# Performance work log

Hardware: AMD Instinct MI355X
Metric: run time of the kernel (lower is better)

## Reference

```python
import jax, jax.numpy as jnp
import numpy as np

S, N, D_IN, D_GNN, E = 8, 50000, 128, 128, 1600000


def setup_inputs() -> dict:
    key = jax.random.key(0)
    k = jax.random.split(key, 7)
    inp = jax.random.normal(k[0], (S, N, D_IN), dtype=jnp.float32)
    edge_index = jax.random.randint(k[1], (2, E), 0, N, dtype=jnp.int64)
    # SAGEConv params: lin_l (neighbor branch, with bias), lin_r (root, no bias)
    s_in = 1.0 / np.sqrt(D_IN)
    W_l = jax.random.uniform(k[2], (D_GNN, D_IN), jnp.float32, -s_in, s_in)
    b_l = jax.random.uniform(k[3], (D_GNN,), jnp.float32, -s_in, s_in)
    W_r = jax.random.uniform(k[4], (D_GNN, D_IN), jnp.float32, -s_in, s_in)
    s_g = 1.0 / np.sqrt(D_GNN)
    W_fc = jax.random.uniform(k[5], (1, D_GNN), jnp.float32, -s_g, s_g)
    b_fc = jax.random.uniform(k[6], (1,), jnp.float32, -s_g, s_g)
    return {"input": inp, "edge_index": edge_index, "W_l": W_l, "b_l": b_l,
            "W_r": W_r, "W_fc": W_fc, "b_fc": b_fc}


def reference(input, edge_index, W_l, b_l, W_r, W_fc, b_fc):
    src, dst = edge_index[0], edge_index[1]
    n = input.shape[1]
    # in-degree for mean aggregation (isolated nodes -> divide by 1, agg stays 0)
    deg = jax.ops.segment_sum(jnp.ones(src.shape[0], input.dtype), dst,
                              num_segments=n)
    deg = jnp.maximum(deg, 1.0)[:, None]

    def step(xt):  # xt: [N, D_IN]
        agg = jax.ops.segment_sum(xt[src], dst, num_segments=n) / deg
        # SAGEConv: lin_l(mean_agg) + lin_r(x)
        return agg @ W_l.T + b_l + xt @ W_r.T  # [N, D_GNN]

    xs = jax.vmap(step)(input)                   # [S, N, D_GNN]
    ys = (xs @ W_fc.T + b_fc)[..., 0]            # [S, N]
    return xs, ys
```

## Files before the change

kernel.cpp:

```cpp
#include <hip/hip_runtime.h>

#define S_STEPS 8
#define D 128

typedef __attribute__((ext_vector_type(4))) float f32x4;
typedef __attribute__((ext_vector_type(4))) short s16x4;
typedef __attribute__((ext_vector_type(8))) short s16x8;

static __device__ __forceinline__ short f2bf(float f) {
    union { float f; unsigned u; } x; x.f = f;
    unsigned r = x.u + 0x7fffu + ((x.u >> 16) & 1u);
    return (short)(r >> 16);
}

__global__ void count_kernel(const int* __restrict__ dst, int* __restrict__ cnt, int E) {
    int e = blockIdx.x * blockDim.x + threadIdx.x;
    if (e < E) atomicAdd(&cnt[dst[e]], 1);
}

__global__ void cvtw_kernel(const float* __restrict__ Wl, const float* __restrict__ Wr,
                            unsigned short* __restrict__ wbf) {
    int i = blockIdx.x * blockDim.x + threadIdx.x;
    if (i < 256 * 128) {
        int j = i >> 7, k = i & 127;
        float v = (j < 128) ? Wl[j * 128 + k] : Wr[(j - 128) * 128 + k];
        wbf[i] = (unsigned short)f2bf(v);
    }
}

__global__ void cvtwcat_kernel(const float* __restrict__ Wl, const float* __restrict__ Wr,
                               unsigned short* __restrict__ wcat) {
    int i = blockIdx.x * blockDim.x + threadIdx.x;
    if (i < 128 * 256) {
        int j = i >> 8, k = i & 255;
        float v = (k < 128) ? Wl[j * 128 + k] : Wr[j * 128 + (k - 128)];
        wcat[i] = (unsigned short)f2bf(v);
    }
}

__global__ __launch_bounds__(256) void cvtx_kernel(const float* __restrict__ x,
    unsigned short* __restrict__ xbfA, unsigned short* __restrict__ xbfB, int N)
{
    const int lane = threadIdx.x & 63;
    const int wv = threadIdx.x >> 6;
    const int node = blockIdx.x * 4 + wv;
    if (node >= N) return;
#pragma unroll
    for (int t = 0; t < S_STEPS; ++t) {
        float2 v = *(const float2*)(x + ((size_t)t * N + node) * 128 + lane * 2);
        ushort2 u;
        u.x = (unsigned short)f2bf(v.x);
        u.y = (unsigned short)f2bf(v.y);
        unsigned short* tb = (t < 4) ? xbfA : xbfB;
        *(ushort2*)(tb + ((size_t)node * 4 + (t & 3)) * 128 + lane * 2) = u;
    }
}

__global__ __launch_bounds__(1024) void scan_kernel(const int* __restrict__ cnt,
                            int* __restrict__ row_ptr,
                            int* __restrict__ fill, float* __restrict__ rdeg,
                            int N, int E) {
    __shared__ int wsum[16];
    __shared__ int woff[16];
    __shared__ int carry_s;
    const int tid = threadIdx.x;
    const int lane = tid & 63;
    const int wv = tid >> 6;
    if (tid == 0) carry_s = 0;
    __syncthreads();
    for (int base = 0; base < N; base += 1024) {
        int i = base + tid;
        int v = (i < N) ? cnt[i] : 0;
        int inc = v;
#pragma unroll
        for (int off = 1; off < 64; off <<= 1) {
            int t = __shfl_up(inc, off);
            if (lane >= off) inc += t;
        }
        if (lane == 63) wsum[wv] = inc;
        __syncthreads();
        if (wv == 0 && lane < 16) {
            int s = wsum[lane];
            int in2 = s;
#pragma unroll
            for (int off = 1; off < 16; off <<= 1) {
                int t = __shfl_up(in2, off);
                if (lane >= off) in2 += t;
            }
            woff[lane] = in2 - s;
        }
        __syncthreads();
        int carry = carry_s;
        int excl = carry + woff[wv] + inc - v;
        if (i < N) {
            row_ptr[i] = excl;
            fill[i] = excl;
            rdeg[i] = 1.0f / (float)((v > 1) ? v : 1);
        }
        __syncthreads();
        if (tid == 1023) carry_s = carry + woff[15] + inc;
        __syncthreads();
    }
    if (tid == 0) row_ptr[N] = E;
}

__global__ void fill_kernel(const int* __restrict__ src, const int* __restrict__ dst,
                            int* __restrict__ fill, int* __restrict__ eidx, int E) {
    int e = blockIdx.x * blockDim.x + threadIdx.x;
    if (e < E) {
        int p = atomicAdd(&fill[dst[e]], 1);
        eidx[p] = src[e];
    }
}

__global__ __launch_bounds__(256) void lin_kernel(const float* __restrict__ x,
    const unsigned short* __restrict__ wbf, const float* __restrict__ bl,
    unsigned short* __restrict__ hbf, float* __restrict__ outb, int N,
    int SF, int tf)
{
    __shared__ __align__(16) short As[64 * 136];
    __shared__ float bls[128];

    const int tid = threadIdx.x;
    const int row0 = blockIdx.x * 64;
    const int lane = tid & 63;
    const int w = tid >> 6;
    const int m = lane & 15;
    const int q = lane >> 4;

    s16x8 bf[4][4];
#pragma unroll
    for (int ct = 0; ct < 4; ++ct) {
#pragma unroll
        for (int kc = 0; kc < 4; ++kc) {
            int col = (w * 4 + ct) * 16 + m;
            bf[ct][kc] = *(const s16x8*)(wbf + (size_t)col * 128 + kc * 32 + q * 8);
        }
    }
    if (tid < 128) bls[tid] = bl[tid];

#pragma unroll
    for (int it = 0; it < 8; ++it) {
        int i = tid + it * 256;
        int r = i >> 5;
        int kq = i & 31;
        int grow = row0 + r;
        float4 v = make_float4(0.f, 0.f, 0.f, 0.f);
        if (grow < N) v = *(const float4*)(x + (size_t)grow * 128 + kq * 4);
        s16x4 a; a.x = f2bf(v.x); a.y = f2bf(v.y); a.z = f2bf(v.z); a.w = f2bf(v.w);
        *(s16x4*)&As[r * 136 + kq * 4] = a;
    }
    __syncthreads();

    f32x4 acc[4][4];
#pragma unroll
    for (int i = 0; i < 4; ++i)
#pragma unroll
        for (int j = 0; j < 4; ++j) acc[i][j] = (f32x4){0.f, 0.f, 0.f, 0.f};

#pragma unroll
    for (int mt = 0; mt < 4; ++mt) {
        s16x8 af[4];
#pragma unroll
        for (int kc = 0; kc < 4; ++kc)
            af[kc] = *(const s16x8*)&As[(mt * 16 + m) * 136 + kc * 32 + q * 8];
#pragma unroll
        for (int ct = 0; ct < 4; ++ct)
#pragma unroll
            for (int kc = 0; kc < 4; ++kc)
                acc[mt][ct] = __builtin_amdgcn_mfma_f32_16x16x32_bf16(
                    af[kc], bf[ct][kc], acc[mt][ct], 0, 0, 0);
    }

    const int colbase = w * 64;
#pragma unroll
    for (int mt = 0; mt < 4; ++mt) {
        const int rowbase = row0 + mt * 16 + q * 4;
#pragma unroll
        for (int ct = 0; ct < 4; ++ct) {
            int col = colbase + ct * 16 + m;
#pragma unroll
            for (int r = 0; r < 4; ++r) {
                int rr = rowbase + r;
                if (rr < N) {
                    if (col < 128) {
                        hbf[((size_t)rr * SF + tf) * 128 + col] =
                            (unsigned short)f2bf(acc[mt][ct][r]);
                    } else {
                        outb[(size_t)rr * 128 + (col - 128)] = acc[mt][ct][r] + bls[col - 128];
                    }
                }
            }
        }
    }
}

#define BF2ACC(u, j) { union { unsigned v; float f; } lo_, hi_; \
    lo_.v = (u) << 16; hi_.v = (u) & 0xffff0000u; \
    acc[j] += lo_.f; acc[(j) + 1] += hi_.f; }
#define ACC8(p, j) { BF2ACC((p).x, (j)); BF2ACC((p).y, (j) + 2); \
    BF2ACC((p).z, (j) + 4); BF2ACC((p).w, (j) + 6); }

__global__ __launch_bounds__(256) void agg4x_kernel(const unsigned short* __restrict__ xbfH,
    const int* __restrict__ row_ptr, const int* __restrict__ eidx,
    const float* __restrict__ rdeg, unsigned short* __restrict__ aggxH, int N)
{
    const int lane = threadIdx.x & 63;
    const int wv = threadIdx.x >> 6;
    const int node = blockIdx.x * 4 + wv;
    if (node >= N) return;

    const int beg = row_ptr[node];
    const int end = row_ptr[node + 1];

    float acc[8];
#pragma unroll
    for (int j = 0; j < 8; ++j) acc[j] = 0.f;

    const uint4* hb = (const uint4*)xbfH;

    int e = beg;
    for (; e + 4 <= end; e += 4) {
        int s0 = eidx[e];
        int s1 = eidx[e + 1];
        int s2 = eidx[e + 2];
        int s3 = eidx[e + 3];
        uint4 a = hb[(size_t)s0 * 64 + lane];
        uint4 b = hb[(size_t)s1 * 64 + lane];
        uint4 c = hb[(size_t)s2 * 64 + lane];
        uint4 d = hb[(size_t)s3 * 64 + lane];
        ACC8(a, 0); ACC8(b, 0); ACC8(c, 0); ACC8(d, 0);
    }
    for (; e < end; ++e) {
        int s0 = eidx[e];
        uint4 a = hb[(size_t)s0 * 64 + lane];
        ACC8(a, 0);
    }

    const float rd = rdeg[node];
    unsigned short* orow = aggxH + ((size_t)node * 4 + (lane >> 4)) * 128 + (lane & 15) * 8;
    s16x8 o;
#pragma unroll
    for (int j = 0; j < 8; ++j) o[j] = f2bf(acc[j] * rd);
    __builtin_nontemporal_store(o, (s16x8*)orow);
}

__global__ __launch_bounds__(256) void lin2_kernel(
    const unsigned short* __restrict__ aggxA, const unsigned short* __restrict__ aggxB,
    const unsigned short* __restrict__ xbfA, const unsigned short* __restrict__ xbfB,
    const unsigned short* __restrict__ wcat, const float* __restrict__ bl,
    const float* __restrict__ wfc, const float* __restrict__ bfc,
    float* __restrict__ xs, float* __restrict__ ys, int N)
{
    __shared__ __align__(16) short As[64 * 264];
    __shared__ float bls[128];
    __shared__ float wfs[128];
    __shared__ float part[4][64];

    const int tid = threadIdx.x;
    const int node0 = blockIdx.x * 8;
    const int lane = tid & 63;
    const int w = tid >> 6;
    const int m = lane & 15;
    const int q = lane >> 4;

    s16x8 bf[2][8];
#pragma unroll
    for (int ct = 0; ct < 2; ++ct) {
#pragma unroll
        for (int kc = 0; kc < 8; ++kc) {
            int col = w * 32 + ct * 16 + m;
            bf[ct][kc] = *(const s16x8*)(wcat + (size_t)col * 256 + kc * 32 + q * 8);
        }
    }
    if (tid < 128) { bls[tid] = bl[tid]; wfs[tid] = wfc[tid]; }

#pragma unroll
    for (int it = 0; it < 4; ++it) {
        int c = tid + it * 256;
        int nl = c >> 7;
        int j = c & 127;
        int t = j >> 4;
        int k16 = j & 15;
        int row = nl * 8 + t;
        int node = node0 + nl;
        s16x8 va = (s16x8){0,0,0,0,0,0,0,0};
        s16x8 vx = (s16x8){0,0,0,0,0,0,0,0};
        if (node < N) {
            const unsigned short* at = (t < 4) ? aggxA : aggxB;
            const unsigned short* xt = (t < 4) ? xbfA : xbfB;
            size_t src = ((size_t)node * 4 + (t & 3)) * 128 + k16 * 8;
            va = *(const s16x8*)(at + src);
            vx = *(const s16x8*)(xt + src);
        }
        *(s16x8*)&As[row * 264 + k16 * 8] = va;
        *(s16x8*)&As[row * 264 + 128 + k16 * 8] = vx;
    }
    __syncthreads();

    f32x4 acc[4][2];
#pragma unroll
    for (int i = 0; i < 4; ++i)
#pragma unroll
        for (int j = 0; j < 2; ++j) acc[i][j] = (f32x4){0.f, 0.f, 0.f, 0.f};

#pragma unroll
    for (int mt = 0; mt < 4; ++mt) {
        s16x8 af[8];
#pragma unroll
        for (int kc = 0; kc < 8; ++kc)
            af[kc] = *(const s16x8*)&As[(mt * 16 + m) * 264 + kc * 32 + q * 8];
#pragma unroll
        for (int ct = 0; ct < 2; ++ct)
#pragma unroll
            for (int kc = 0; kc < 8; ++kc)
                acc[mt][ct] = __builtin_amdgcn_mfma_f32_16x16x32_bf16(
                    af[kc], bf[ct][kc], acc[mt][ct], 0, 0, 0);
    }

    float pd[4][4];
#pragma unroll
    for (int i = 0; i < 4; ++i)
#pragma unroll
        for (int r = 0; r < 4; ++r) pd[i][r] = 0.f;

    const int colb = w * 32;
#pragma unroll
    for (int mt = 0; mt < 4; ++mt) {
#pragma unroll
        for (int ct = 0; ct < 2; ++ct) {
            int col = colb + ct * 16 + m;
            float blv = bls[col];
            float wfv = wfs[col];
#pragma unroll
            for (int r = 0; r < 4; ++r) {
                int row = mt * 16 + q * 4 + r;
                int node = node0 + (row >> 3);
                int t = row & 7;
                float o = acc[mt][ct][r] + blv;
                if (node < N) xs[((size_t)t * N + node) * 128 + col] = o;
                pd[mt][r] += o * wfv;
            }
        }
    }
#pragma unroll
    for (int off = 1; off < 16; off <<= 1)
#pragma unroll
        for (int mt = 0; mt < 4; ++mt)
#pragma unroll
            for (int r = 0; r < 4; ++r)
                pd[mt][r] += __shfl_xor(pd[mt][r], off);
    if (m == 0) {
#pragma unroll
        for (int mt = 0; mt < 4; ++mt)
#pragma unroll
            for (int r = 0; r < 4; ++r)
                part[w][mt * 16 + q * 4 + r] = pd[mt][r];
    }
    __syncthreads();
    if (tid < 64) {
        int row = tid;
        float v = part[0][row] + part[1][row] + part[2][row] + part[3][row] + bfc[0];
        int node = node0 + (row >> 3);
        int t = row & 7;
        if (node < N) ys[(size_t)t * N + node] = v;
    }
}

__global__ __launch_bounds__(256) void agg_kernel(const unsigned short* __restrict__ hbf,
    const int* __restrict__ row_ptr, const int* __restrict__ eidx,
    const float* __restrict__ rdeg, const float* __restrict__ wfc,
    const float* __restrict__ bfc, float* __restrict__ outb,
    float* __restrict__ ys, int N)
{
    const int lane = threadIdx.x & 63;
    const int wv = threadIdx.x >> 6;
    const int node = blockIdx.x * 4 + wv;
    if (node >= N) return;
    const int g = lane >> 4;
    const int l = lane & 15;
    const int beg = row_ptr[node];
    const int end = row_ptr[node + 1];

    float acc[8];
#pragma unroll
    for (int j = 0; j < 8; ++j) acc[j] = 0.f;

    const unsigned short* hb = hbf + l * 8;
#pragma unroll 2
    for (int e = beg + g; e < end; e += 4) {
        int s = eidx[e];
        uint4 pk = *(const uint4*)(hb + (size_t)s * 128);
        union { unsigned u; float f; } t;
        t.u = pk.x << 16;        acc[0] += t.f;
        t.u = pk.x & 0xffff0000u; acc[1] += t.f;
        t.u = pk.y << 16;        acc[2] += t.f;
        t.u = pk.y & 0xffff0000u; acc[3] += t.f;
        t.u = pk.z << 16;        acc[4] += t.f;
        t.u = pk.z & 0xffff0000u; acc[5] += t.f;
        t.u = pk.w << 16;        acc[6] += t.f;
        t.u = pk.w & 0xffff0000u; acc[7] += t.f;
    }
#pragma unroll
    for (int j = 0; j < 8; ++j) {
        acc[j] += __shfl_xor(acc[j], 16);
        acc[j] += __shfl_xor(acc[j], 32);
    }
    float ax = (g == 0) ? acc[0] : (g == 1) ? acc[2] : (g == 2) ? acc[4] : acc[6];
    float ay = (g == 0) ? acc[1] : (g == 1) ? acc[3] : (g == 2) ? acc[5] : acc[7];

    const int feat = l * 8 + g * 2;
    const float rd = rdeg[node];
    const float2 base = *(const float2*)(outb + (size_t)node * 128 + feat);
    float ox = base.x + ax * rd;
    float oy = base.y + ay * rd;
    *(float2*)(outb + (size_t)node * 128 + feat) = make_float2(ox, oy);

    const float2 wv2 = *(const float2*)(wfc + feat);
    float p = ox * wv2.x + oy * wv2.y;
#pragma unroll
    for (int off = 32; off > 0; off >>= 1) p += __shfl_down(p, off);
    if (lane == 0) ys[node] = p + bfc[0];
}

extern "C" void kernel_launch(void* const* d_in, const int* in_sizes, int n_in,
                              void* d_out, int out_size, void* d_ws, size_t ws_size,
                              hipStream_t stream)
{
    const float* x   = (const float*)d_in[0];
    const int*   ei  = (const int*)d_in[1];
    const float* Wl  = (const float*)d_in[2];
    const float* bl  = (const float*)d_in[3];
    const float* Wr  = (const float*)d_in[4];
    const float* Wfc = (const float*)d_in[5];
    const float* bfc = (const float*)d_in[6];

    const int N = in_sizes[0] / (S_STEPS * D);
    const int E = in_sizes[1] / 2;
    const int* srcp = ei;
    const int* dstp = ei + E;

    char* p = (char*)d_ws;
    auto alloc = [&](size_t bytes) {
        char* r = p;
        p += (bytes + 255) & ~(size_t)255;
        return r;
    };
    int*   cnt     = (int*)alloc((size_t)N * 4);
    int*   row_ptr = (int*)alloc((size_t)(N + 1) * 4);
    int*   fill    = (int*)alloc((size_t)N * 4);
    float* rdeg    = (float*)alloc((size_t)N * 4);
    int*   eidx    = (int*)alloc((size_t)E * 4);
    unsigned short* wmat = (unsigned short*)alloc((size_t)256 * 128 * 2);

    size_t used = (size_t)(p - (char*)d_ws);
    size_t htbl = (size_t)N * 4 * D * 2;
    bool v5 = (ws_size >= used + 4 * htbl + 4096);

    float* xs    = (float*)d_out;
    float* ysall = xs + (size_t)S_STEPS * N * D;

    (void)hipMemsetAsync(cnt, 0, (size_t)N * 4, stream);
    count_kernel<<<(E + 255) / 256, 256, 0, stream>>>(dstp, cnt, E);
    scan_kernel<<<1, 1024, 0, stream>>>(cnt, row_ptr, fill, rdeg, N, E);
    fill_kernel<<<(E + 255) / 256, 256, 0, stream>>>(srcp, dstp, fill, eidx, E);

    if (v5) {
        unsigned short* xbfA  = (unsigned short*)alloc(htbl);
        unsigned short* xbfB  = (unsigned short*)alloc(htbl);
        unsigned short* aggxA = (unsigned short*)alloc(htbl);
        unsigned short* aggxB = (unsigned short*)alloc(htbl);
        cvtwcat_kernel<<<128, 256, 0, stream>>>(Wl, Wr, wmat);
        cvtx_kernel<<<(N + 3) / 4, 256, 0, stream>>>(x, xbfA, xbfB, N);
        agg4x_kernel<<<(N + 3) / 4, 256, 0, stream>>>(xbfA, row_ptr, eidx, rdeg,
                                                      aggxA, N);
        agg4x_kernel<<<(N + 3) / 4, 256, 0, stream>>>(xbfB, row_ptr, eidx, rdeg,
                                                      aggxB, N);
        lin2_kernel<<<(N + 7) / 8, 256, 0, stream>>>(aggxA, aggxB, xbfA, xbfB,
                                                     wmat, bl, Wfc, bfc,
                                                     xs, ysall, N);
    } else {
        unsigned short* hbf = (unsigned short*)alloc((size_t)N * D * 2);
        cvtw_kernel<<<128, 256, 0, stream>>>(Wl, Wr, wmat);
        const int gl = (N + 63) / 64;
        const int ga = (N + 3) / 4;
        for (int t = 0; t < S_STEPS; ++t) {
            const float* xt = x + (size_t)t * N * D;
            float* outb = xs + (size_t)t * N * D;
            lin_kernel<<<gl, 256, 0, stream>>>(xt, wmat, bl, hbf, outb, N, 1, 0);
            agg_kernel<<<ga, 256, 0, stream>>>(hbf, row_ptr, eidx, rdeg, Wfc, bfc,
                                               outb, ysall + (size_t)t * N, N);
        }
    }
}
```

Measured before the change: 1.122 ms.

## Build CSR with two-level bucket radix sort instead of global atomics

Replaces the count/scan/fill CSR construction (per-node global atomics plus a single-block serial scan over N) with a two-pass bucket sort. Edges are histogrammed into 256-node buckets, scattered into a packed buffer using block-local atomics, and then sorted within each bucket in shared memory, which also writes row_ptr. Degree reciprocals are now computed from row_ptr inside the aggregation kernel rather than read from a separate array. The path is taken only when NB<256 and N<2^24, and it needs an extra E-sized buffer.

```diff
diff --git a/kernel.cpp b/kernel.cpp
--- a/kernel.cpp
+++ b/kernel.cpp
@@ -13,47 +13,119 @@
     return (short)(r >> 16);
 }
 
+
+__global__ __launch_bounds__(256) void bhist_kernel(const int* __restrict__ dst,
+    int* __restrict__ bhist, int E)
+{
+    __shared__ int lh[256];
+    lh[threadIdx.x] = 0;
+    __syncthreads();
+    for (int e = blockIdx.x * 256 + threadIdx.x; e < E; e += gridDim.x * 256)
+        atomicAdd(&lh[dst[e] >> 8], 1);
+    __syncthreads();
+    int v = lh[threadIdx.x];
+    if (v) atomicAdd(&bhist[threadIdx.x], v);
+}
+
+__global__ __launch_bounds__(256) void bscan_kernel(const int* __restrict__ bhist,
+    int* __restrict__ bbase, int* __restrict__ cursor, int* __restrict__ row_ptr,
+    int N, int E, int NB)
+{
+    __shared__ int wsum[4];
+    __shared__ int woff[4];
+    const int tid = threadIdx.x;
+    const int lane = tid & 63;
+    const int wv = tid >> 6;
+    int v = (tid < NB) ? bhist[tid] : 0;
+    int inc = v;
+#pragma unroll
+    for (int off = 1; off < 64; off <<= 1) {
+        int t = __shfl_up(inc, off);
+        if (lane >= off) inc += t;
+    }
+    if (lane == 63) wsum[wv] = inc;
+    __syncthreads();
+    if (tid == 0) { int s = 0; for (int k = 0; k < 4; ++k) { woff[k] = s; s += wsum[k]; } }
+    __syncthreads();
+    int excl = woff[wv] + inc - v;
+    if (tid < NB) { bbase[tid] = excl; cursor[tid] = excl; }
+    if (tid == NB) bbase[NB] = E;
+    if (tid == 0) row_ptr[N] = E;
+}
+
+__global__ __launch_bounds__(256) void scat_kernel(const int* __restrict__ src,
+    const int* __restrict__ dst, int* __restrict__ cursor,
+    unsigned* __restrict__ ebuf, int E, int len, int NB)
+{
+    __shared__ int lh[256];
+    __shared__ int lb[256];
+    const int tid = threadIdx.x;
+    const int e0 = blockIdx.x * len;
+    const int e1 = min(E, e0 + len);
+    if (e0 >= E) return;
+    lh[tid] = 0;
+    __syncthreads();
+    for (int e = e0 + tid; e < e1; e += 256)
+        atomicAdd(&lh[dst[e] >> 8], 1);
+    __syncthreads();
+    if (tid < NB) lb[tid] = lh[tid] ? atomicAdd(&cursor[tid], lh[tid]) : 0;
+    __syncthreads();
+    lh[tid] = 0;
+    __syncthreads();
+    for (int e = e0 + tid; e < e1; e += 256) {
+        int d = dst[e];
+        int b = d >> 8;
+        int off = atomicAdd(&lh[b], 1);
+        ebuf[lb[b] + off] = ((unsigned)src[e] << 8) | (unsigned)(d & 255);
+    }
+}
+
+__global__ __launch_bounds__(256) void bsort_kernel(const unsigned* __restrict__ ebuf,
+    const int* __restrict__ bbase, int* __restrict__ row_ptr,
+    int* __restrict__ eidx, int N)
+{
+    __shared__ int cnt[256];
+    __shared__ int wsum[4];
+    __shared__ int woff[4];
+    const int tid = threadIdx.x;
+    const int b = blockIdx.x;
+    const int base = bbase[b];
+    const int K = bbase[b + 1] - base;
+    cnt[tid] = 0;
+    __syncthreads();
+    for (int i = tid; i < K; i += 256)
+        atomicAdd(&cnt[ebuf[base + i] & 255], 1);
+    __syncthreads();
+    int v = cnt[tid];
+    int inc = v;
+    const int lane = tid & 63;
+    const int wv = tid >> 6;
+#pragma unroll
+    for (int off = 1; off < 64; off <<= 1) {
+        int t = __shfl_up(inc, off);
+        if (lane >= off) inc += t;
+    }
+    if (lane == 63) wsum[wv] = inc;
+    __syncthreads();
+    if (tid == 0) { int s = 0; for (int k = 0; k < 4; ++k) { woff[k] = s; s += wsum[k]; } }
+    __syncthreads();
+    int excl = woff[wv] + inc - v;
+    int node = b * 256 + tid;
+    if (node < N) row_ptr[node] = base + excl;
+    __syncthreads();
+    cnt[tid] = excl;
+    __syncthreads();
+    for (int i = tid; i < K; i += 256) {
+        unsigned u = ebuf[base + i];
+        int off = atomicAdd(&cnt[u & 255], 1);
+        eidx[base + off] = (int)(u >> 8);
+    }
+}
+
+
 __global__ void count_kernel(const int* __restrict__ dst, int* __restrict__ cnt, int E) {
     int e = blockIdx.x * blockDim.x + threadIdx.x;
     if (e < E) atomicAdd(&cnt[dst[e]], 1);
-}
-
-__global__ void cvtw_kernel(const float* __restrict__ Wl, const float* __restrict__ Wr,
-                            unsigned short* __restrict__ wbf) {
-    int i = blockIdx.x * blockDim.x + threadIdx.x;
-    if (i < 256 * 128) {
-        int j = i >> 7, k = i & 127;
-        float v = (j < 128) ? Wl[j * 128 + k] : Wr[(j - 128) * 128 + k];
-        wbf[i] = (unsigned short)f2bf(v);
-    }
-}
-
-__global__ void cvtwcat_kernel(const float* __restrict__ Wl, const float* __restrict__ Wr,
-                               unsigned short* __restrict__ wcat) {
-    int i = blockIdx.x * blockDim.x + threadIdx.x;
-    if (i < 128 * 256) {
-        int j = i >> 8, k = i & 255;
-        float v = (k < 128) ? Wl[j * 128 + k] : Wr[j * 128 + (k - 128)];
-        wcat[i] = (unsigned short)f2bf(v);
-    }
-}
-
-__global__ __launch_bounds__(256) void cvtx_kernel(const float* __restrict__ x,
-    unsigned short* __restrict__ xbfA, unsigned short* __restrict__ xbfB, int N)
-{
-    const int lane = threadIdx.x & 63;
-    const int wv = threadIdx.x >> 6;
-    const int node = blockIdx.x * 4 + wv;
-    if (node >= N) return;
-#pragma unroll
-    for (int t = 0; t < S_STEPS; ++t) {
-        float2 v = *(const float2*)(x + ((size_t)t * N + node) * 128 + lane * 2);
-        ushort2 u;
-        u.x = (unsigned short)f2bf(v.x);
-        u.y = (unsigned short)f2bf(v.y);
-        unsigned short* tb = (t < 4) ? xbfA : xbfB;
-        *(ushort2*)(tb + ((size_t)node * 4 + (t & 3)) * 128 + lane * 2) = u;
-    }
 }
 
 __global__ __launch_bounds__(1024) void scan_kernel(const int* __restrict__ cnt,
@@ -113,6 +185,46 @@
     }
 }
 
+
+__global__ void cvtw_kernel(const float* __restrict__ Wl, const float* __restrict__ Wr,
+                            unsigned short* __restrict__ wbf) {
+    int i = blockIdx.x * blockDim.x + threadIdx.x;
+    if (i < 256 * 128) {
+        int j = i >> 7, k = i & 127;
+        float v = (j < 128) ? Wl[j * 128 + k] : Wr[(j - 128) * 128 + k];
+        wbf[i] = (unsigned short)f2bf(v);
+    }
+}
+
+__global__ void cvtwcat_kernel(const float* __restrict__ Wl, const float* __restrict__ Wr,
+                               unsigned short* __restrict__ wcat) {
+    int i = blockIdx.x * blockDim.x + threadIdx.x;
+    if (i < 128 * 256) {
+        int j = i >> 8, k = i & 255;
+        float v = (k < 128) ? Wl[j * 128 + k] : Wr[j * 128 + (k - 128)];
+        wcat[i] = (unsigned short)f2bf(v);
+    }
+}
+
+__global__ __launch_bounds__(256) void cvtx_kernel(const float* __restrict__ x,
+    unsigned short* __restrict__ xbfA, unsigned short* __restrict__ xbfB, int N)
+{
+    const int lane = threadIdx.x & 63;
+    const int wv = threadIdx.x >> 6;
+    const int node = blockIdx.x * 4 + wv;
+    if (node >= N) return;
+#pragma unroll
+    for (int t = 0; t < S_STEPS; ++t) {
+        float2 v = *(const float2*)(x + ((size_t)t * N + node) * 128 + lane * 2);
+        ushort2 u;
+        u.x = (unsigned short)f2bf(v.x);
+        u.y = (unsigned short)f2bf(v.y);
+        unsigned short* tb = (t < 4) ? xbfA : xbfB;
+        *(ushort2*)(tb + ((size_t)node * 4 + (t & 3)) * 128 + lane * 2) = u;
+    }
+}
+
+
 __global__ __launch_bounds__(256) void lin_kernel(const float* __restrict__ x,
     const unsigned short* __restrict__ wbf, const float* __restrict__ bl,
     unsigned short* __restrict__ hbf, float* __restrict__ outb, int N,
@@ -203,7 +315,7 @@
 
 __global__ __launch_bounds__(256) void agg4x_kernel(const unsigned short* __restrict__ xbfH,
     const int* __restrict__ row_ptr, const int* __restrict__ eidx,
-    const float* __restrict__ rdeg, unsigned short* __restrict__ aggxH, int N)
+    unsigned short* __restrict__ aggxH, int N)
 {
     const int lane = threadIdx.x & 63;
     const int wv = threadIdx.x >> 6;
@@ -237,7 +349,8 @@
         ACC8(a, 0);
     }
 
-    const float rd = rdeg[node];
+    int deg = end - beg;
+    const float rd = 1.0f / (float)((deg > 1) ? deg : 1);
     unsigned short* orow = aggxH + ((size_t)node * 4 + (lane >> 4)) * 128 + (lane & 15) * 8;
     s16x8 o;
 #pragma unroll
@@ -446,41 +559,54 @@
         p += (bytes + 255) & ~(size_t)255;
         return r;
     };
-    int*   cnt     = (int*)alloc((size_t)N * 4);
     int*   row_ptr = (int*)alloc((size_t)(N + 1) * 4);
-    int*   fill    = (int*)alloc((size_t)N * 4);
-    float* rdeg    = (float*)alloc((size_t)N * 4);
     int*   eidx    = (int*)alloc((size_t)E * 4);
     unsigned short* wmat = (unsigned short*)alloc((size_t)256 * 128 * 2);
 
+    const int NB = (N + 255) >> 8;
     size_t used = (size_t)(p - (char*)d_ws);
     size_t htbl = (size_t)N * 4 * D * 2;
-    bool v5 = (ws_size >= used + 4 * htbl + 4096);
+    size_t radix = ((size_t)E * 4 + 256) + 3 * ((size_t)(NB + 1) * 4 + 256);
+    bool v6 = (NB >= 1) && (NB < 256) && (N < (1 << 24)) &&
+              (ws_size >= used + radix + 4 * htbl + 65536);
 
     float* xs    = (float*)d_out;
     float* ysall = xs + (size_t)S_STEPS * N * D;
 
-    (void)hipMemsetAsync(cnt, 0, (size_t)N * 4, stream);
-    count_kernel<<<(E + 255) / 256, 256, 0, stream>>>(dstp, cnt, E);
-    scan_kernel<<<1, 1024, 0, stream>>>(cnt, row_ptr, fill, rdeg, N, E);
-    fill_kernel<<<(E + 255) / 256, 256, 0, stream>>>(srcp, dstp, fill, eidx, E);
-
-    if (v5) {
+    if (v6) {
+        unsigned* ebuf = (unsigned*)alloc((size_t)E * 4);
+        int* bhist  = (int*)alloc((size_t)(NB + 1) * 4);
+        int* bbase  = (int*)alloc((size_t)(NB + 1) * 4);
+        int* cursor = (int*)alloc((size_t)(NB + 1) * 4);
         unsigned short* xbfA  = (unsigned short*)alloc(htbl);
         unsigned short* xbfB  = (unsigned short*)alloc(htbl);
         unsigned short* aggxA = (unsigned short*)alloc(htbl);
         unsigned short* aggxB = (unsigned short*)alloc(htbl);
+
+        (void)hipMemsetAsync(bhist, 0, (size_t)NB * 4, stream);
+        bhist_kernel<<<384, 256, 0, stream>>>(dstp, bhist, E);
+        bscan_kernel<<<1, 256, 0, stream>>>(bhist, bbase, cursor, row_ptr, N, E, NB);
+        const int len = (E + 511) / 512;
+        scat_kernel<<<512, 256, 0, stream>>>(srcp, dstp, cursor, ebuf, E, len, NB);
+        bsort_kernel<<<NB, 256, 0, stream>>>(ebuf, bbase, row_ptr, eidx, N);
+
         cvtwcat_kernel<<<128, 256, 0, stream>>>(Wl, Wr, wmat);
         cvtx_kernel<<<(N + 3) / 4, 256, 0, stream>>>(x, xbfA, xbfB, N);
-        agg4x_kernel<<<(N + 3) / 4, 256, 0, stream>>>(xbfA, row_ptr, eidx, rdeg,
-                                                      aggxA, N);
-        agg4x_kernel<<<(N + 3) / 4, 256, 0, stream>>>(xbfB, row_ptr, eidx, rdeg,
-                                                      aggxB, N);
+        agg4x_kernel<<<(N + 3) / 4, 256, 0, stream>>>(xbfA, row_ptr, eidx, aggxA, N);
+        agg4x_kernel<<<(N + 3) / 4, 256, 0, stream>>>(xbfB, row_ptr, eidx, aggxB, N);
         lin2_kernel<<<(N + 7) / 8, 256, 0, stream>>>(aggxA, aggxB, xbfA, xbfB,
                                                      wmat, bl, Wfc, bfc,
                                                      xs, ysall, N);
     } else {
+        int*   cnt  = (int*)alloc((size_t)N * 4);
+        int*   fill = (int*)alloc((size_t)N * 4);
+        float* rdeg = (float*)alloc((size_t)N * 4);
         unsigned short* hbf = (unsigned short*)alloc((size_t)N * D * 2);
+
+        (void)hipMemsetAsync(cnt, 0, (size_t)N * 4, stream);
+        count_kernel<<<(E + 255) / 256, 256, 0, stream>>>(dstp, cnt, E);
+        scan_kernel<<<1, 1024, 0, stream>>>(cnt, row_ptr, fill, rdeg, N, E);
+        fill_kernel<<<(E + 255) / 256, 256, 0, stream>>>(srcp, dstp, fill, eidx, E);
         cvtw_kernel<<<128, 256, 0, stream>>>(Wl, Wr, wmat);
         const int gl = (N + 63) / 64;
         const int ga = (N + 3) / 4;
```

Measured after the change: 953.9 us. -15.0%, faster.
